# Kernel tuning notes

Hardware: AMD Instinct MI355X
Metric: run time of the kernel (lower is better)

The kernel has to match this reference:

```python
import jax, jax.numpy as jnp
import numpy as np

N_NODES = 50000
N_EDGES = 1048576
NODE_H = 128
EDGE_H = 64
GNN_H = 128


def setup_inputs() -> dict:
    key = jax.random.key(0)
    k = jax.random.split(key, 6)
    x = jax.random.normal(k[0], (N_NODES, NODE_H), dtype=jnp.float32)
    edge_index = jax.random.randint(k[1], (2, N_EDGES), 0, N_NODES, dtype=jnp.int64)
    edge_attr = jax.random.normal(k[2], (N_EDGES, EDGE_H), dtype=jnp.float32)
    # kaiming-ish init for the two Linear layers
    W1 = jax.random.normal(k[3], (2 * NODE_H + EDGE_H, GNN_H), dtype=jnp.float32) * (2.0 / (2 * NODE_H + EDGE_H)) ** 0.5
    b1 = jnp.zeros((GNN_H,), dtype=jnp.float32)
    W2 = jax.random.normal(k[4], (NODE_H + GNN_H, GNN_H), dtype=jnp.float32) * (2.0 / (NODE_H + GNN_H)) ** 0.5
    b2 = jnp.zeros((GNN_H,), dtype=jnp.float32)
    return {"x": x, "edge_index": edge_index, "edge_attr": edge_attr,
            "W1": W1, "b1": b1, "W2": W2, "b2": b2}


def reference(x, edge_index, edge_attr, W1, b1, W2, b2):
    # GroupGNN_Layer.forward
    row, col = edge_index[0], edge_index[1]
    n = x.shape[0]
    # gather + concat + edge MLP (Linear -> ReLU)
    msg = jnp.concatenate([x[row], x[col], edge_attr], axis=1)  # [E, 2*node_h+edge_h]
    msg = jax.nn.relu(msg @ W1 + b1)                            # [E, gnn_h]
    # scatter_mean over target nodes (col), dim_size = n
    s = jax.ops.segment_sum(msg, col, num_segments=n)           # [N, gnn_h]
    cnt = jax.ops.segment_sum(jnp.ones((msg.shape[0],), msg.dtype), col, num_segments=n)
    agg = s / jnp.maximum(cnt, 1.0)[:, None]                    # empty segments -> 0
    # node MLP (Linear -> ReLU)
    out = jax.nn.relu(jnp.concatenate([x, agg], axis=1) @ W2 + b2)  # [N, gnn_h]
    return out
```

## Files before the change

kernel.cpp:

```cpp
#include <hip/hip_runtime.h>
#include <hip/hip_bf16.h>
#include <stdint.h>

#define E_EDGES 1048576
#define NN 50000
#define NODE_H 128
#define EDGE_H 64
#define GNN_H 128
#define K1 320
#define K2 256
#define NB 16
#define NG (NN / NB)
#define CAPN 64

typedef __bf16 bf16_t;
typedef __bf16 bf16x8 __attribute__((ext_vector_type(8)));
typedef float floatx4 __attribute__((ext_vector_type(4)));

#define OFF_FLAG 0
#define OFF_CNT 256
#define OFF_W1T 213248
#define OFF_W2T 295168
#define OFF_W1ABT 360704
#define OFF_W1CT 426240
#define OFF_RC 442880
#define OFF_REC 26042880
#define WS_V13 ((size_t)OFF_REC + (size_t)NN * CAPN * 8)

__device__ __forceinline__ long load_idx(const void* ei, int is64, long off) {
    return is64 ? (long)((const long long*)ei)[off] : (long)((const int*)ei)[off];
}
__device__ __forceinline__ float bflo(unsigned u) {
    return __builtin_bit_cast(float, u << 16);
}
__device__ __forceinline__ float bfhi(unsigned u) {
    return __builtin_bit_cast(float, u & 0xffff0000u);
}

#define MFMA(a, b, c) __builtin_amdgcn_mfma_f32_16x16x32_bf16(a, b, c, 0, 0, 0)


__global__ __launch_bounds__(256) void prep_w(const float* __restrict__ W1,
                                              const float* __restrict__ W2,
                                              char* __restrict__ ws) {
    bf16_t* w2t = (bf16_t*)(ws + OFF_W2T);
    bf16_t* w1abt = (bf16_t*)(ws + OFF_W1ABT);
    bf16_t* w1ct = (bf16_t*)(ws + OFF_W1CT);
    int tid = blockIdx.x * 256 + threadIdx.x;
    int nt = 64 * 256;
    for (int i = tid; i < K2 * GNN_H; i += nt) {
        int n = i / K2, k = i - n * K2;
        w2t[i] = (bf16_t)W2[k * GNN_H + n];
    }
    for (int i = tid; i < 256 * 128; i += nt) {
        int n = i >> 7, k = i & 127;
        int kk = (n < 128) ? k : k + 128;
        w1abt[i] = (bf16_t)W1[kk * GNN_H + (n & 127)];
    }
    for (int i = tid; i < 128 * 64; i += nt) {
        int n = i >> 6, k = i & 63;
        w1ct[i] = (bf16_t)W1[(256 + k) * GNN_H + n];
    }
}

__global__ __launch_bounds__(256) void scatrc_kernel(const int* __restrict__ ei32,
                                                     const float* __restrict__ x,
                                                     char* __restrict__ ws,
                                                     int* __restrict__ cnt) {
    if (blockIdx.x < E_EDGES / 256) {
        __shared__ int nz;
        int tid = threadIdx.x;
        int e = blockIdx.x * 256 + tid;
        if (tid == 0) nz = 0;
        __syncthreads();
        if (ei32[2 * e + 1] != 0) atomicOr(&nz, 1);
        __syncthreads();
        int is64 = (nz == 0);
        const long long* e64 = (const long long*)ei32;
        int row = is64 ? (int)e64[e] : ei32[e];
        int col = is64 ? (int)e64[E_EDGES + e] : ei32[E_EDGES + e];
        int pos = atomicAdd(cnt + col, 1);
        if (pos < CAPN)
            ((unsigned long long*)(ws + OFF_REC))[((size_t)col << 6) + pos] =
                (unsigned long long)(unsigned)e |
                ((unsigned long long)(unsigned)row << 20);
    } else {
        const bf16_t* w1abt = (const bf16_t*)(ws + OFF_W1ABT);
        bf16_t* rc = (bf16_t*)(ws + OFF_RC);
        int lane = threadIdx.x & 63;
        int w = threadIdx.x >> 6;
        int li = lane & 15;
        int h = lane >> 4;
        int m0 = (blockIdx.x - E_EDGES / 256) * 16;

        bf16x8 bf[4][4];
#pragma unroll
        for (int t = 0; t < 4; ++t)
#pragma unroll
            for (int ks = 0; ks < 4; ++ks)
                bf[t][ks] = *(const bf16x8*)(w1abt + (w * 64 + t * 16 + li) * 128 + ks * 32 + h * 8);

        const float* px = x + (long)(m0 + li) * NODE_H + h * 8;
        floatx4 acc[4] = {{0.f, 0.f, 0.f, 0.f}, {0.f, 0.f, 0.f, 0.f},
                          {0.f, 0.f, 0.f, 0.f}, {0.f, 0.f, 0.f, 0.f}};
#pragma unroll
        for (int ks = 0; ks < 4; ++ks) {
            floatx4 f0 = *(const floatx4*)(px + ks * 32);
            floatx4 f1 = *(const floatx4*)(px + ks * 32 + 4);
            bf16x8 a;
#pragma unroll
            for (int j = 0; j < 4; ++j) {
                a[j] = (bf16_t)f0[j];
                a[j + 4] = (bf16_t)f1[j];
            }
#pragma unroll
            for (int t = 0; t < 4; ++t) acc[t] = MFMA(a, bf[t][ks], acc[t]);
        }
#pragma unroll
        for (int t = 0; t < 4; ++t) {
            int base = w * 64 + t * 16;
            int ppos;
            if (base < 128)
                ppos = (base >> 5) * 32 + li * 2 + ((base >> 4) & 1);
            else
                ppos = base + li;
#pragma unroll
            for (int r = 0; r < 4; ++r)
                rc[(long)(m0 + 4 * h + r) * 256 + ppos] = (bf16_t)acc[t][r];
        }
    }
}

__global__ __launch_bounds__(256) void fused_v14(
    const float* __restrict__ x, const float* __restrict__ ea,
    const float* __restrict__ b1, const float* __restrict__ b2,
    const char* __restrict__ ws, float* __restrict__ out) {
    const bf16_t* w1ct = (const bf16_t*)(ws + OFF_W1CT);
    const bf16_t* w2t = (const bf16_t*)(ws + OFF_W2T);
    const bf16_t* rc = (const bf16_t*)(ws + OFF_RC);
    const char* rcb = (const char*)rc;
    const int* cnt = (const int*)(ws + OFF_CNT);
    const unsigned long long* rec = (const unsigned long long*)(ws + OFF_REC);

    __shared__ float agg[NB][132];
    __shared__ float cl[NB][132];
    __shared__ int scnt[NB];
    __shared__ int offs[NB + 1];
    __shared__ unsigned lrec_e[NB * CAPN];
    __shared__ unsigned lrec_p[NB * CAPN];

    int tid = threadIdx.x;
    int lane = tid & 63;
    int w = tid >> 6;
    int li = lane & 15;
    int h = lane >> 4;
    int h4 = h * 4;
    int c0 = w * 32;
    int roff = w * 64 + li * 4;
    int v0 = blockIdx.x * NB;

    for (int i = tid; i < NB * 132; i += 256) ((float*)agg)[i] = 0.f;
    {
        int j = tid >> 4;
        int cc = (tid & 15) * 8;
        bf16x8 v = *(const bf16x8*)(rc + (long)(v0 + j) * 256 + 128 + cc);
#pragma unroll
        for (int q = 0; q < 8; ++q) cl[j][cc + q] = (float)v[q] + b1[cc + q];
    }
    if (tid < NB) {
        int c = cnt[v0 + tid];
        scnt[tid] = c > CAPN ? CAPN : c;
    }
    __syncthreads();
    if (tid == 0) {
        int run = 0;
#pragma unroll
        for (int j = 0; j < NB; ++j) {
            offs[j] = run;
            run += scnt[j];
        }
        offs[NB] = run;
    }
    __syncthreads();
    for (int flat = tid; flat < NB * CAPN; flat += 256) {
        int j = flat >> 6, i = flat & 63;
        if (i < scnt[j]) {
            unsigned long long r = rec[((size_t)(v0 + j) << 6) + i];
            int d = offs[j] + i;
            lrec_e[d] = (unsigned)r & 0xFFFFFu;
            lrec_p[d] = ((unsigned)(r >> 20) & 0x1FFFFu) | ((unsigned)j << 17);
        }
    }

    bf16x8 bc00 = *(const bf16x8*)(w1ct + (c0 + li) * 64 + h * 8);
    bf16x8 bc01 = *(const bf16x8*)(w1ct + (c0 + li) * 64 + 32 + h * 8);
    bf16x8 bc10 = *(const bf16x8*)(w1ct + (c0 + 16 + li) * 64 + h * 8);
    bf16x8 bc11 = *(const bf16x8*)(w1ct + (c0 + 16 + li) * 64 + 32 + h * 8);
    __syncthreads();

    int n_e = offs[NB];
    if (n_e > 0) {
        const int ntile = (n_e + 15) >> 4;
#define CP(p) ((p) < n_e ? (p) : n_e - 1)
#define DECL_SET(S)                                                     \
    unsigned pe##S, pk##S##0, pk##S##1, pk##S##2, pk##S##3, nlp##S;     \
    floatx4 ea##S##0, ea##S##1, ea##S##2, ea##S##3;                     \
    unsigned rp##S##0, rp##S##1, rp##S##2, rp##S##3;
#define IDX(S, T)                                                       \
    do {                                                                \
        int bb_ = (T) << 4;                                             \
        pe##S = lrec_e[CP(bb_ + li)];                                   \
        pk##S##0 = lrec_p[CP(bb_ + h4)];                                \
        pk##S##1 = lrec_p[CP(bb_ + h4 + 1)];                            \
        pk##S##2 = lrec_p[CP(bb_ + h4 + 2)];                            \
        pk##S##3 = lrec_p[CP(bb_ + h4 + 3)];                            \
    } while (0)
#define DATA(S)                                                         \
    do {                                                                \
        const float* pe_ = ea + (size_t)pe##S * EDGE_H + h * 8;         \
        ea##S##0 = *(const floatx4*)(pe_);                              \
        ea##S##1 = *(const floatx4*)(pe_ + 4);                          \
        ea##S##2 = *(const floatx4*)(pe_ + 32);                         \
        ea##S##3 = *(const floatx4*)(pe_ + 36);                         \
        rp##S##0 = *(const unsigned*)(rcb + (((size_t)(pk##S##0 & 0x1FFFFu)) << 9) + roff); \
        rp##S##1 = *(const unsigned*)(rcb + (((size_t)(pk##S##1 & 0x1FFFFu)) << 9) + roff); \
        rp##S##2 = *(const unsigned*)(rcb + (((size_t)(pk##S##2 & 0x1FFFFu)) << 9) + roff); \
        rp##S##3 = *(const unsigned*)(rcb + (((size_t)(pk##S##3 & 0x1FFFFu)) << 9) + roff); \
        nlp##S = ((pk##S##0 >> 17) & 15u) | (((pk##S##1 >> 17) & 15u) << 4) | \
                 (((pk##S##2 >> 17) & 15u) << 8) |                      \
                 (((pk##S##3 >> 17) & 15u) << 12);                      \
    } while (0)
#define COMPUTE(S, T)                                                   \
    do {                                                                \
        bf16x8 a0_, a1_;                                                \
        _Pragma("unroll") for (int j_ = 0; j_ < 4; ++j_) {              \
            a0_[j_] = (bf16_t)ea##S##0[j_];                             \
            a0_[j_ + 4] = (bf16_t)ea##S##1[j_];                         \
            a1_[j_] = (bf16_t)ea##S##2[j_];                             \
            a1_[j_ + 4] = (bf16_t)ea##S##3[j_];                         \
        }                                                               \
        floatx4 ac0_ = {0.f, 0.f, 0.f, 0.f};                            \
        floatx4 ac1_ = {0.f, 0.f, 0.f, 0.f};                            \
        ac0_ = MFMA(a0_, bc00, ac0_);                                   \
        ac0_ = MFMA(a1_, bc01, ac0_);                                   \
        ac1_ = MFMA(a0_, bc10, ac1_);                                   \
        ac1_ = MFMA(a1_, bc11, ac1_);                                   \
        int base_ = (T) << 4;                                           \
        int nl0_ = (int)(nlp##S & 15u);                                 \
        int nl1_ = (int)((nlp##S >> 4) & 15u);                          \
        int nl2_ = (int)((nlp##S >> 8) & 15u);                          \
        int nl3_ = (int)((nlp##S >> 12) & 15u);                         \
        float m00_ = fmaxf(ac0_[0] + bflo(rp##S##0) + cl[nl0_][c0 + li], 0.f); \
        float m01_ = fmaxf(ac0_[1] + bflo(rp##S##1) + cl[nl1_][c0 + li], 0.f); \
        float m02_ = fmaxf(ac0_[2] + bflo(rp##S##2) + cl[nl2_][c0 + li], 0.f); \
        float m03_ = fmaxf(ac0_[3] + bflo(rp##S##3) + cl[nl3_][c0 + li], 0.f); \
        float m10_ = fmaxf(ac1_[0] + bfhi(rp##S##0) + cl[nl0_][c0 + 16 + li], 0.f); \
        float m11_ = fmaxf(ac1_[1] + bfhi(rp##S##1) + cl[nl1_][c0 + 16 + li], 0.f); \
        float m12_ = fmaxf(ac1_[2] + bfhi(rp##S##2) + cl[nl2_][c0 + 16 + li], 0.f); \
        float m13_ = fmaxf(ac1_[3] + bfhi(rp##S##3) + cl[nl3_][c0 + 16 + li], 0.f); \
        if ((base_ + h4 + 3) < n_e && nl0_ == nl3_) {                   \
            atomicAdd(&agg[nl0_][c0 + li], m00_ + m01_ + m02_ + m03_);  \
            atomicAdd(&agg[nl0_][c0 + 16 + li], m10_ + m11_ + m12_ + m13_); \
        } else {                                                        \
            if (base_ + h4 < n_e) {                                     \
                atomicAdd(&agg[nl0_][c0 + li], m00_);                   \
                atomicAdd(&agg[nl0_][c0 + 16 + li], m10_);              \
            }                                                           \
            if (base_ + h4 + 1 < n_e) {                                 \
                atomicAdd(&agg[nl1_][c0 + li], m01_);                   \
                atomicAdd(&agg[nl1_][c0 + 16 + li], m11_);              \
            }                                                           \
            if (base_ + h4 + 2 < n_e) {                                 \
                atomicAdd(&agg[nl2_][c0 + li], m02_);                   \
                atomicAdd(&agg[nl2_][c0 + 16 + li], m12_);              \
            }                                                           \
            if (base_ + h4 + 3 < n_e) {                                 \
                atomicAdd(&agg[nl3_][c0 + li], m03_);                   \
                atomicAdd(&agg[nl3_][c0 + 16 + li], m13_);              \
            }                                                           \
        }                                                               \
    } while (0)

        DECL_SET(A)
        DECL_SET(B)
        IDX(A, 0);
        IDX(B, 1);
        DATA(A);
        DATA(B);
        IDX(A, 2);
        IDX(B, 3);
        for (int t = 0; t < ntile; t += 2) {
            COMPUTE(A, t);
            DATA(A);
            IDX(A, t + 4);
            COMPUTE(B, t + 1);
            DATA(B);
            IDX(B, t + 5);
        }
#undef CP
    }
    __syncthreads();

    bf16x8 bfr2[2][8];
#pragma unroll
    for (int t = 0; t < 2; ++t)
#pragma unroll
        for (int ks = 0; ks < 8; ++ks)
            bfr2[t][ks] = *(const bf16x8*)(w2t + (long)(c0 + t * 16 + li) * K2 + ks * 32 + h * 8);
    float nb0 = b2[c0 + li];
    float nb1 = b2[c0 + 16 + li];

    int node = v0 + li;
    float rcn = 1.0f / fmaxf((float)cnt[node], 1.0f);
    const float* px = x + (long)node * NODE_H + h * 8;
    floatx4 acc0 = {0.f, 0.f, 0.f, 0.f};
    floatx4 acc1 = {0.f, 0.f, 0.f, 0.f};
#pragma unroll
    for (int ks = 0; ks < 8; ++ks) {
        floatx4 f0, f1;
        if (ks < 4) {
            f0 = *(const floatx4*)(px + ks * 32);
            f1 = *(const floatx4*)(px + ks * 32 + 4);
        } else {
            const float* sa = &agg[li][(ks - 4) * 32 + h * 8];
            f0 = *(const floatx4*)(sa);
            f1 = *(const floatx4*)(sa + 4);
            f0 *= rcn;
            f1 *= rcn;
        }
        bf16x8 a;
#pragma unroll
        for (int j = 0; j < 4; ++j) {
            a[j] = (bf16_t)f0[j];
            a[j + 4] = (bf16_t)f1[j];
        }
        acc0 = MFMA(a, bfr2[0][ks], acc0);
        acc1 = MFMA(a, bfr2[1][ks], acc1);
    }
#pragma unroll
    for (int r = 0; r < 4; ++r) {
        long ir = v0 + h4 + r;
        out[ir * GNN_H + c0 + li] = fmaxf(acc0[r] + nb0, 0.f);
        out[ir * GNN_H + c0 + 16 + li] = fmaxf(acc1[r] + nb1, 0.f);
    }
}


__global__ void prep_kernel(const float* __restrict__ W1, const float* __restrict__ W2,
                            const int* __restrict__ ei32, char* __restrict__ ws) {
    bf16_t* w1t = (bf16_t*)(ws + OFF_W1T);
    bf16_t* w2t = (bf16_t*)(ws + OFF_W2T);
    int tid = blockIdx.x * blockDim.x + threadIdx.x;
    int nt = gridDim.x * blockDim.x;
    for (int i = tid; i < K1 * GNN_H; i += nt) {
        int n = i / K1, k = i - n * K1;
        w1t[i] = (bf16_t)W1[k * GNN_H + n];
    }
    for (int i = tid; i < K2 * GNN_H; i += nt) {
        int n = i / K2, k = i - n * K2;
        w2t[i] = (bf16_t)W2[k * GNN_H + n];
    }
    if (blockIdx.x == 0) {
        __shared__ int any_nonzero;
        if (threadIdx.x == 0) any_nonzero = 0;
        __syncthreads();
        if (ei32[2 * threadIdx.x + 1] != 0) atomicOr(&any_nonzero, 1);
        __syncthreads();
        if (threadIdx.x == 0) *(int*)(ws + OFF_FLAG) = (any_nonzero == 0) ? 1 : 0;
    }
}

__global__ void count_kernel(const void* __restrict__ ei, const char* __restrict__ ws,
                             float* __restrict__ cnt) {
    int is64 = *(const int*)(ws + OFF_FLAG);
    int e = blockIdx.x * blockDim.x + threadIdx.x;
    if (e < E_EDGES) {
        long c = load_idx(ei, is64, (long)E_EDGES + e);
        atomicAdd(cnt + c, 1.0f);
    }
}

__global__ __launch_bounds__(256) void edge_kernel(
    const float* __restrict__ x, const void* __restrict__ ei,
    const float* __restrict__ ea, const float* __restrict__ b1,
    const char* __restrict__ ws, float* __restrict__ s) {
    const bf16_t* w1t = (const bf16_t*)(ws + OFF_W1T);
    int is64 = *(const int*)(ws + OFF_FLAG);
    int lane = threadIdx.x & 63;
    int w = threadIdx.x >> 6;
    int li = lane & 15;
    int h = lane >> 4;
    int n0 = w * 32;

    bf16x8 bf[2][10];
#pragma unroll
    for (int t = 0; t < 2; ++t)
#pragma unroll
        for (int ks = 0; ks < 10; ++ks)
            bf[t][ks] = *(const bf16x8*)(w1t + (long)(n0 + t * 16 + li) * K1 + ks * 32 + h * 8);
    float bias0 = b1[n0 + li];
    float bias1 = b1[n0 + 16 + li];

    const int ntiles = E_EDGES / 16;
    for (int tile = blockIdx.x; tile < ntiles; tile += gridDim.x) {
        int m0 = tile * 16;
        int e = m0 + li;
        long rowi = load_idx(ei, is64, e);
        long coli = load_idx(ei, is64, (long)E_EDGES + e);
        const float* pr = x + rowi * NODE_H + h * 8;
        const float* pc = x + coli * NODE_H + h * 8;
        const float* pe = ea + (long)e * EDGE_H + h * 8;
        floatx4 acc0 = {0.f, 0.f, 0.f, 0.f};
        floatx4 acc1 = {0.f, 0.f, 0.f, 0.f};
#pragma unroll
        for (int ks = 0; ks < 10; ++ks) {
            const float* src = (ks < 4) ? (pr + ks * 32) : (ks < 8) ? (pc + (ks - 4) * 32)
                                                                    : (pe + (ks - 8) * 32);
            floatx4 f0 = *(const floatx4*)(src);
            floatx4 f1 = *(const floatx4*)(src + 4);
            bf16x8 a;
#pragma unroll
            for (int j = 0; j < 4; ++j) {
                a[j] = (bf16_t)f0[j];
                a[j + 4] = (bf16_t)f1[j];
            }
            acc0 = MFMA(a, bf[0][ks], acc0);
            acc1 = MFMA(a, bf[1][ks], acc1);
        }
        long cols[4];
#pragma unroll
        for (int r = 0; r < 4; ++r)
            cols[r] = load_idx(ei, is64, (long)E_EDGES + m0 + h * 4 + r);
#pragma unroll
        for (int r = 0; r < 4; ++r) {
            float v0 = fmaxf(acc0[r] + bias0, 0.f);
            float v1 = fmaxf(acc1[r] + bias1, 0.f);
            atomicAdd(s + cols[r] * GNN_H + n0 + li, v0);
            atomicAdd(s + cols[r] * GNN_H + n0 + 16 + li, v1);
        }
    }
}

__global__ __launch_bounds__(256) void node_kernel(
    const float* __restrict__ x, const float* __restrict__ b2,
    const char* __restrict__ ws, const float* __restrict__ cnt,
    const float* __restrict__ s, float* __restrict__ out) {
    const bf16_t* w2t = (const bf16_t*)(ws + OFF_W2T);
    int lane = threadIdx.x & 63;
    int w = threadIdx.x >> 6;
    int li = lane & 15;
    int h = lane >> 4;
    int n0 = w * 32;

    bf16x8 bf[2][8];
#pragma unroll
    for (int t = 0; t < 2; ++t)
#pragma unroll
        for (int ks = 0; ks < 8; ++ks)
            bf[t][ks] = *(const bf16x8*)(w2t + (long)(n0 + t * 16 + li) * K2 + ks * 32 + h * 8);
    float bias0 = b2[n0 + li];
    float bias1 = b2[n0 + 16 + li];

    int m0 = blockIdx.x * 16;
    int i = m0 + li;
    float rcn = 1.0f / fmaxf(cnt[i], 1.0f);
    const float* px = x + (long)i * NODE_H + h * 8;
    const float* ps = s + (long)i * GNN_H + h * 8;
    floatx4 acc0 = {0.f, 0.f, 0.f, 0.f};
    floatx4 acc1 = {0.f, 0.f, 0.f, 0.f};
#pragma unroll
    for (int ks = 0; ks < 8; ++ks) {
        const float* src = (ks < 4) ? (px + ks * 32) : (ps + (ks - 4) * 32);
        floatx4 f0 = *(const floatx4*)(src);
        floatx4 f1 = *(const floatx4*)(src + 4);
        if (ks >= 4) {
            f0 *= rcn;
            f1 *= rcn;
        }
        bf16x8 a;
#pragma unroll
        for (int j = 0; j < 4; ++j) {
            a[j] = (bf16_t)f0[j];
            a[j + 4] = (bf16_t)f1[j];
        }
        acc0 = MFMA(a, bf[0][ks], acc0);
        acc1 = MFMA(a, bf[1][ks], acc1);
    }
    __syncthreads();
#pragma unroll
    for (int r = 0; r < 4; ++r) {
        long ir = m0 + h * 4 + r;
        out[ir * GNN_H + n0 + li] = fmaxf(acc0[r] + bias0, 0.f);
        out[ir * GNN_H + n0 + 16 + li] = fmaxf(acc1[r] + bias1, 0.f);
    }
}

extern "C" void kernel_launch(void* const* d_in, const int* in_sizes, int n_in,
                              void* d_out, int out_size, void* d_ws, size_t ws_size,
                              hipStream_t stream) {
    const float* x = (const float*)d_in[0];
    const void* ei = d_in[1];
    const float* ea = (const float*)d_in[2];
    const float* W1 = (const float*)d_in[3];
    const float* b1 = (const float*)d_in[4];
    const float* W2 = (const float*)d_in[5];
    const float* b2 = (const float*)d_in[6];
    float* out = (float*)d_out;
    char* ws = (char*)d_ws;

    if (ws_size >= WS_V13) {
        int* cnt = (int*)(ws + OFF_CNT);
        hipMemsetAsync(cnt, 0, NN * 4, stream);
        prep_w<<<64, 256, 0, stream>>>(W1, W2, ws);
        scatrc_kernel<<<E_EDGES / 256 + NG, 256, 0, stream>>>((const int*)ei, x, ws, cnt);
        fused_v14<<<NG, 256, 0, stream>>>(x, ea, b1, b2, ws, out);
    } else {
        prep_kernel<<<32, 256, 0, stream>>>(W1, W2, (const int*)ei, ws);
        float* cntf = (float*)(ws + OFF_CNT);
        hipMemsetAsync(cntf, 0, NN * 4, stream);
        hipMemsetAsync(out, 0, (size_t)NN * GNN_H * 4, stream);
        count_kernel<<<E_EDGES / 256, 256, 0, stream>>>(ei, ws, cntf);
        edge_kernel<<<4096, 256, 0, stream>>>(x, ei, ea, b1, ws, out);
        node_kernel<<<NN / 16, 256, 0, stream>>>(x, b2, ws, cntf, out, out);
    }
}
```

Baseline: 408.6 us.

## Stream edge attributes into LDS via direct global-to-LDS loads with ring buffer

Replaces per-lane register loads of edge_attr rows with __builtin_amdgcn_global_load_lds into a four-slot shared-memory ring, staged four tiles ahead. Reads go back out of LDS with a rotated column layout to avoid bank conflicts. This is meant to cut vector register pressure and issue more loads in flight for the random-gather edge stream. In exchange it adds two workgroup barriers per tile and hand-set vmcnt waits, which depend on the exact count of outstanding loads and are fragile.

```diff
diff --git a/kernel.cpp b/kernel.cpp
--- a/kernel.cpp
+++ b/kernel.cpp
@@ -131,7 +131,7 @@
     }
 }
 
-__global__ __launch_bounds__(256) void fused_v14(
+__global__ __launch_bounds__(256) void fused_v15(
     const float* __restrict__ x, const float* __restrict__ ea,
     const float* __restrict__ b1, const float* __restrict__ b2,
     const char* __restrict__ ws, float* __restrict__ out) {
@@ -148,6 +148,7 @@
     __shared__ int offs[NB + 1];
     __shared__ unsigned lrec_e[NB * CAPN];
     __shared__ unsigned lrec_p[NB * CAPN];
+    __shared__ float eabuf[4][16][64];
 
     int tid = threadIdx.x;
     int lane = tid & 63;
@@ -201,55 +202,56 @@
     int n_e = offs[NB];
     if (n_e > 0) {
         const int ntile = (n_e + 15) >> 4;
-#define CP(p) ((p) < n_e ? (p) : n_e - 1)
-#define DECL_SET(S)                                                     \
-    unsigned pe##S, pk##S##0, pk##S##1, pk##S##2, pk##S##3, nlp##S;     \
-    floatx4 ea##S##0, ea##S##1, ea##S##2, ea##S##3;                     \
-    unsigned rp##S##0, rp##S##1, rp##S##2, rp##S##3;
-#define IDX(S, T)                                                       \
-    do {                                                                \
-        int bb_ = (T) << 4;                                             \
-        pe##S = lrec_e[CP(bb_ + li)];                                   \
-        pk##S##0 = lrec_p[CP(bb_ + h4)];                                \
-        pk##S##1 = lrec_p[CP(bb_ + h4 + 1)];                            \
-        pk##S##2 = lrec_p[CP(bb_ + h4 + 2)];                            \
-        pk##S##3 = lrec_p[CP(bb_ + h4 + 3)];                            \
+        int jj = (w << 2) + (lane >> 4);
+        unsigned ebrot = (unsigned)(((lane & 15) * 16 + ((jj & 7) << 5)) & 255);
+        int c0r = ((h << 3) - ((li & 7) << 3)) & 63;
+        int c1r = (c0r + 32) & 63;
+
+#define CPm(p) ((p) < 0 ? 0 : ((p) < n_e ? (p) : n_e - 1))
+#define DECL_SET(S) unsigned rp##S##0, rp##S##1, rp##S##2, rp##S##3, nlp##S;
+#define STAGE(T)                                                            \
+    do {                                                                    \
+        unsigned e_ = lrec_e[CPm(((T) << 4) + jj)];                         \
+        const char* g_ = (const char*)ea + ((size_t)e_ << 8) + ebrot;       \
+        __builtin_amdgcn_global_load_lds(                                   \
+            (const __attribute__((address_space(1))) void*)g_,              \
+            (__attribute__((address_space(3))) void*)&eabuf[(T) & 3][w << 2][0], \
+            16, 0, 0);                                                      \
     } while (0)
-#define DATA(S)                                                         \
-    do {                                                                \
-        const float* pe_ = ea + (size_t)pe##S * EDGE_H + h * 8;         \
-        ea##S##0 = *(const floatx4*)(pe_);                              \
-        ea##S##1 = *(const floatx4*)(pe_ + 4);                          \
-        ea##S##2 = *(const floatx4*)(pe_ + 32);                         \
-        ea##S##3 = *(const floatx4*)(pe_ + 36);                         \
-        rp##S##0 = *(const unsigned*)(rcb + (((size_t)(pk##S##0 & 0x1FFFFu)) << 9) + roff); \
-        rp##S##1 = *(const unsigned*)(rcb + (((size_t)(pk##S##1 & 0x1FFFFu)) << 9) + roff); \
-        rp##S##2 = *(const unsigned*)(rcb + (((size_t)(pk##S##2 & 0x1FFFFu)) << 9) + roff); \
-        rp##S##3 = *(const unsigned*)(rcb + (((size_t)(pk##S##3 & 0x1FFFFu)) << 9) + roff); \
-        nlp##S = ((pk##S##0 >> 17) & 15u) | (((pk##S##1 >> 17) & 15u) << 4) | \
-                 (((pk##S##2 >> 17) & 15u) << 8) |                      \
-                 (((pk##S##3 >> 17) & 15u) << 12);                      \
+#define DATA_R(S, T)                                                        \
+    do {                                                                    \
+        int bb_ = (T) << 4;                                                 \
+        unsigned k0_ = lrec_p[CPm(bb_ + h4)];                               \
+        unsigned k1_ = lrec_p[CPm(bb_ + h4 + 1)];                           \
+        unsigned k2_ = lrec_p[CPm(bb_ + h4 + 2)];                           \
+        unsigned k3_ = lrec_p[CPm(bb_ + h4 + 3)];                           \
+        rp##S##0 = *(const unsigned*)(rcb + (((size_t)(k0_ & 0x1FFFFu)) << 9) + roff); \
+        rp##S##1 = *(const unsigned*)(rcb + (((size_t)(k1_ & 0x1FFFFu)) << 9) + roff); \
+        rp##S##2 = *(const unsigned*)(rcb + (((size_t)(k2_ & 0x1FFFFu)) << 9) + roff); \
+        rp##S##3 = *(const unsigned*)(rcb + (((size_t)(k3_ & 0x1FFFFu)) << 9) + roff); \
+        nlp##S = ((k0_ >> 17) & 15u) | (((k1_ >> 17) & 15u) << 4) |         \
+                 (((k2_ >> 17) & 15u) << 8) | (((k3_ >> 17) & 15u) << 12);  \
     } while (0)
-#define COMPUTE(S, T)                                                   \
-    do {                                                                \
-        bf16x8 a0_, a1_;                                                \
-        _Pragma("unroll") for (int j_ = 0; j_ < 4; ++j_) {              \
-            a0_[j_] = (bf16_t)ea##S##0[j_];                             \
-            a0_[j_ + 4] = (bf16_t)ea##S##1[j_];                         \
-            a1_[j_] = (bf16_t)ea##S##2[j_];                             \
-            a1_[j_ + 4] = (bf16_t)ea##S##3[j_];                         \
-        }                                                               \
-        floatx4 ac0_ = {0.f, 0.f, 0.f, 0.f};                            \
-        floatx4 ac1_ = {0.f, 0.f, 0.f, 0.f};                            \
-        ac0_ = MFMA(a0_, bc00, ac0_);                                   \
-        ac0_ = MFMA(a1_, bc01, ac0_);                                   \
-        ac1_ = MFMA(a0_, bc10, ac1_);                                   \
-        ac1_ = MFMA(a1_, bc11, ac1_);                                   \
-        int base_ = (T) << 4;                                           \
-        int nl0_ = (int)(nlp##S & 15u);                                 \
-        int nl1_ = (int)((nlp##S >> 4) & 15u);                          \
-        int nl2_ = (int)((nlp##S >> 8) & 15u);                          \
-        int nl3_ = (int)((nlp##S >> 12) & 15u);                         \
+#define COMPUTE(S, T, F0, F1, F2, F3)                                       \
+    do {                                                                    \
+        bf16x8 a0_, a1_;                                                    \
+        _Pragma("unroll") for (int j_ = 0; j_ < 4; ++j_) {                  \
+            a0_[j_] = (bf16_t)F0[j_];                                       \
+            a0_[j_ + 4] = (bf16_t)F1[j_];                                   \
+            a1_[j_] = (bf16_t)F2[j_];                                       \
+            a1_[j_ + 4] = (bf16_t)F3[j_];                                   \
+        }                                                                   \
+        floatx4 ac0_ = {0.f, 0.f, 0.f, 0.f};                                \
+        floatx4 ac1_ = {0.f, 0.f, 0.f, 0.f};                                \
+        ac0_ = MFMA(a0_, bc00, ac0_);                                       \
+        ac0_ = MFMA(a1_, bc01, ac0_);                                       \
+        ac1_ = MFMA(a0_, bc10, ac1_);                                       \
+        ac1_ = MFMA(a1_, bc11, ac1_);                                       \
+        int base_ = (T) << 4;                                               \
+        int nl0_ = (int)(nlp##S & 15u);                                     \
+        int nl1_ = (int)((nlp##S >> 4) & 15u);                              \
+        int nl2_ = (int)((nlp##S >> 8) & 15u);                              \
+        int nl3_ = (int)((nlp##S >> 12) & 15u);                             \
         float m00_ = fmaxf(ac0_[0] + bflo(rp##S##0) + cl[nl0_][c0 + li], 0.f); \
         float m01_ = fmaxf(ac0_[1] + bflo(rp##S##1) + cl[nl1_][c0 + li], 0.f); \
         float m02_ = fmaxf(ac0_[2] + bflo(rp##S##2) + cl[nl2_][c0 + li], 0.f); \
@@ -258,46 +260,53 @@
         float m11_ = fmaxf(ac1_[1] + bfhi(rp##S##1) + cl[nl1_][c0 + 16 + li], 0.f); \
         float m12_ = fmaxf(ac1_[2] + bfhi(rp##S##2) + cl[nl2_][c0 + 16 + li], 0.f); \
         float m13_ = fmaxf(ac1_[3] + bfhi(rp##S##3) + cl[nl3_][c0 + 16 + li], 0.f); \
-        if ((base_ + h4 + 3) < n_e && nl0_ == nl3_) {                   \
-            atomicAdd(&agg[nl0_][c0 + li], m00_ + m01_ + m02_ + m03_);  \
+        if ((base_ + h4 + 3) < n_e && nl0_ == nl3_) {                       \
+            atomicAdd(&agg[nl0_][c0 + li], m00_ + m01_ + m02_ + m03_);      \
             atomicAdd(&agg[nl0_][c0 + 16 + li], m10_ + m11_ + m12_ + m13_); \
-        } else {                                                        \
-            if (base_ + h4 < n_e) {                                     \
-                atomicAdd(&agg[nl0_][c0 + li], m00_);                   \
-                atomicAdd(&agg[nl0_][c0 + 16 + li], m10_);              \
-            }                                                           \
-            if (base_ + h4 + 1 < n_e) {                                 \
-                atomicAdd(&agg[nl1_][c0 + li], m01_);                   \
-                atomicAdd(&agg[nl1_][c0 + 16 + li], m11_);              \
-            }                                                           \
-            if (base_ + h4 + 2 < n_e) {                                 \
-                atomicAdd(&agg[nl2_][c0 + li], m02_);                   \
-                atomicAdd(&agg[nl2_][c0 + 16 + li], m12_);              \
-            }                                                           \
-            if (base_ + h4 + 3 < n_e) {                                 \
-                atomicAdd(&agg[nl3_][c0 + li], m03_);                   \
-                atomicAdd(&agg[nl3_][c0 + 16 + li], m13_);              \
-            }                                                           \
-        }                                                               \
+        } else {                                                            \
+            if (base_ + h4 < n_e) {                                         \
+                atomicAdd(&agg[nl0_][c0 + li], m00_);                       \
+                atomicAdd(&agg[nl0_][c0 + 16 + li], m10_);                  \
+            }                                                               \
+            if (base_ + h4 + 1 < n_e) {                                     \
+                atomicAdd(&agg[nl1_][c0 + li], m01_);                       \
+                atomicAdd(&agg[nl1_][c0 + 16 + li], m11_);                  \
+            }                                                               \
+            if (base_ + h4 + 2 < n_e) {                                     \
+                atomicAdd(&agg[nl2_][c0 + li], m02_);                       \
+                atomicAdd(&agg[nl2_][c0 + 16 + li], m12_);                  \
+            }                                                               \
+            if (base_ + h4 + 3 < n_e) {                                     \
+                atomicAdd(&agg[nl3_][c0 + li], m03_);                       \
+                atomicAdd(&agg[nl3_][c0 + 16 + li], m13_);                  \
+            }                                                               \
+        }                                                                   \
+    } while (0)
+#define HALF(S, TT)                                                         \
+    do {                                                                    \
+        asm volatile("s_waitcnt vmcnt(19)" ::: "memory");                   \
+        __builtin_amdgcn_s_barrier();                                       \
+        __builtin_amdgcn_sched_barrier(0);                                  \
+        const float* rp_ = &eabuf[(TT) & 3][li][0];                         \
+        floatx4 f0_ = *(const floatx4*)(rp_ + c0r);                         \
+        floatx4 f1_ = *(const floatx4*)(rp_ + c0r + 4);                     \
+        floatx4 f2_ = *(const floatx4*)(rp_ + c1r);                         \
+        floatx4 f3_ = *(const floatx4*)(rp_ + c1r + 4);                     \
+        asm volatile("s_waitcnt lgkmcnt(0)" ::: "memory");                  \
+        __builtin_amdgcn_sched_barrier(0);                                  \
+        __builtin_amdgcn_s_barrier();                                       \
+        STAGE((TT) + 4);                                                    \
+        if ((TT) >= 0) COMPUTE(S, TT, f0_, f1_, f2_, f3_);                  \
+        DATA_R(S, (TT) + 2);                                                \
     } while (0)
 
         DECL_SET(A)
         DECL_SET(B)
-        IDX(A, 0);
-        IDX(B, 1);
-        DATA(A);
-        DATA(B);
-        IDX(A, 2);
-        IDX(B, 3);
-        for (int t = 0; t < ntile; t += 2) {
-            COMPUTE(A, t);
-            DATA(A);
-            IDX(A, t + 4);
-            COMPUTE(B, t + 1);
-            DATA(B);
-            IDX(B, t + 5);
-        }
-#undef CP
+        for (int t = -4; t < ntile; t += 2) {
+            HALF(A, t);
+            HALF(B, t + 1);
+        }
+#undef CPm
     }
     __syncthreads();
 
@@ -513,7 +522,7 @@
         hipMemsetAsync(cnt, 0, NN * 4, stream);
         prep_w<<<64, 256, 0, stream>>>(W1, W2, ws);
         scatrc_kernel<<<E_EDGES / 256 + NG, 256, 0, stream>>>((const int*)ei, x, ws, cnt);
-        fused_v14<<<NG, 256, 0, stream>>>(x, ea, b1, b2, ws, out);
+        fused_v15<<<NG, 256, 0, stream>>>(x, ea, b1, b2, ws, out);
     } else {
         prep_kernel<<<32, 256, 0, stream>>>(W1, W2, (const int*)ei, ws);
         float* cntf = (float*)(ws + OFF_CNT);
```

Result: slower. 497.1 us (+21.6%).

## Build CSR via histogram+scan and pre-sort edge_attr as bf16 by target

Applied to the files above, without the earlier changes.

Replaces the fixed-capacity per-node bucket (64 slots) with a proper CSR: a histogram pass, a single-block prefix scan, then a scatter that writes row indices and a bf16 copy of edge_attr in target-sorted order. The fused kernel then reads edge attributes contiguously as bf16 instead of gathering fp32 rows by edge id, and finds each edge's local node by binary search over offsets. This adds an extra histogram pass over the edge list, a serial single-block scan, and a full extra write and read of the bf16 edge attributes.

```diff
diff --git a/kernel.cpp b/kernel.cpp
--- a/kernel.cpp
+++ b/kernel.cpp
@@ -11,7 +11,7 @@
 #define K2 256
 #define NB 16
 #define NG (NN / NB)
-#define CAPN 64
+#define LCAP 1024
 
 typedef __bf16 bf16_t;
 typedef __bf16 bf16x8 __attribute__((ext_vector_type(8)));
@@ -19,13 +19,16 @@
 
 #define OFF_FLAG 0
 #define OFF_CNT 256
-#define OFF_W1T 213248
-#define OFF_W2T 295168
-#define OFF_W1ABT 360704
-#define OFF_W1CT 426240
-#define OFF_RC 442880
-#define OFF_REC 26042880
-#define WS_V13 ((size_t)OFF_REC + (size_t)NN * CAPN * 8)
+#define OFF_RP 200448
+#define OFF_WOFF 400640
+#define OFF_W2T 600832
+#define OFF_W1ABT 666368
+#define OFF_W1CT 731904
+#define OFF_W1T 748288
+#define OFF_RC 830464
+#define OFF_ROW 26430464
+#define OFF_EAB 30624768
+#define WS_V16 ((size_t)OFF_EAB + (size_t)E_EDGES * 128)
 
 __device__ __forceinline__ long load_idx(const void* ei, int is64, long off) {
     return is64 ? (long)((const long long*)ei)[off] : (long)((const int*)ei)[off];
@@ -40,33 +43,79 @@
 #define MFMA(a, b, c) __builtin_amdgcn_mfma_f32_16x16x32_bf16(a, b, c, 0, 0, 0)
 
 
-__global__ __launch_bounds__(256) void prep_w(const float* __restrict__ W1,
-                                              const float* __restrict__ W2,
-                                              char* __restrict__ ws) {
+__global__ __launch_bounds__(256) void prep_hist(const float* __restrict__ W1,
+                                                 const float* __restrict__ W2,
+                                                 const int* __restrict__ ei32,
+                                                 char* __restrict__ ws,
+                                                 int* __restrict__ cnt) {
+    __shared__ int nz;
+    int tid = threadIdx.x;
+    int gid = blockIdx.x * 256 + tid;
+    if (tid == 0) nz = 0;
+    __syncthreads();
+    if (ei32[2 * gid + 1] != 0) atomicOr(&nz, 1);
+    __syncthreads();
+    int is64 = (nz == 0);
+
     bf16_t* w2t = (bf16_t*)(ws + OFF_W2T);
     bf16_t* w1abt = (bf16_t*)(ws + OFF_W1ABT);
     bf16_t* w1ct = (bf16_t*)(ws + OFF_W1CT);
-    int tid = blockIdx.x * 256 + threadIdx.x;
-    int nt = 64 * 256;
-    for (int i = tid; i < K2 * GNN_H; i += nt) {
-        int n = i / K2, k = i - n * K2;
-        w2t[i] = (bf16_t)W2[k * GNN_H + n];
-    }
-    for (int i = tid; i < 256 * 128; i += nt) {
-        int n = i >> 7, k = i & 127;
+    if (gid < K2 * GNN_H) {
+        int n = gid / K2, k = gid - n * K2;
+        w2t[gid] = (bf16_t)W2[k * GNN_H + n];
+    }
+    if (gid < 256 * 128) {
+        int n = gid >> 7, k = gid & 127;
         int kk = (n < 128) ? k : k + 128;
-        w1abt[i] = (bf16_t)W1[kk * GNN_H + (n & 127)];
-    }
-    for (int i = tid; i < 128 * 64; i += nt) {
-        int n = i >> 6, k = i & 63;
-        w1ct[i] = (bf16_t)W1[(256 + k) * GNN_H + n];
-    }
+        w1abt[gid] = (bf16_t)W1[kk * GNN_H + (n & 127)];
+    }
+    if (gid < 128 * 64) {
+        int n = gid >> 6, k = gid & 63;
+        w1ct[gid] = (bf16_t)W1[(256 + k) * GNN_H + n];
+    }
+    if (gid == 0) *(int*)(ws + OFF_FLAG) = is64;
+
+    const long long* e64 = (const long long*)ei32;
+    for (int e = gid; e < E_EDGES; e += 2048 * 256) {
+        int col = is64 ? (int)e64[E_EDGES + e] : ei32[E_EDGES + e];
+        atomicAdd(cnt + col, 1);
+    }
+}
+
+__global__ __launch_bounds__(1024) void scan_kernel(const int* __restrict__ cnt,
+                                                    int* __restrict__ rowptr,
+                                                    int* __restrict__ woff) {
+    __shared__ int part[1024];
+    int t = threadIdx.x;
+    const int CH = (NN + 1023) / 1024;
+    int base = t * CH;
+    int n = NN - base;
+    if (n < 0) n = 0;
+    if (n > CH) n = CH;
+    int s = 0;
+    for (int i = 0; i < n; ++i) s += cnt[base + i];
+    part[t] = s;
+    __syncthreads();
+    for (int off = 1; off < 1024; off <<= 1) {
+        int v = (t >= off) ? part[t - off] : 0;
+        __syncthreads();
+        part[t] += v;
+        __syncthreads();
+    }
+    int run = part[t] - s;
+    for (int i = 0; i < n; ++i) {
+        rowptr[base + i] = run;
+        woff[base + i] = run;
+        run += cnt[base + i];
+    }
+    if (t == 1023) rowptr[NN] = part[1023];
 }
 
 __global__ __launch_bounds__(256) void scatrc_kernel(const int* __restrict__ ei32,
+                                                     const float* __restrict__ ea,
                                                      const float* __restrict__ x,
                                                      char* __restrict__ ws,
-                                                     int* __restrict__ cnt) {
+                                                     int* __restrict__ woff) {
     if (blockIdx.x < E_EDGES / 256) {
         __shared__ int nz;
         int tid = threadIdx.x;
@@ -79,11 +128,22 @@
         const long long* e64 = (const long long*)ei32;
         int row = is64 ? (int)e64[e] : ei32[e];
         int col = is64 ? (int)e64[E_EDGES + e] : ei32[E_EDGES + e];
-        int pos = atomicAdd(cnt + col, 1);
-        if (pos < CAPN)
-            ((unsigned long long*)(ws + OFF_REC))[((size_t)col << 6) + pos] =
-                (unsigned long long)(unsigned)e |
-                ((unsigned long long)(unsigned)row << 20);
+        int pos = atomicAdd(woff + col, 1);
+        ((unsigned*)(ws + OFF_ROW))[pos] = (unsigned)row;
+        const floatx4* src = (const floatx4*)(ea + (size_t)e * EDGE_H);
+        bf16_t* dst = (bf16_t*)(ws + OFF_EAB) + ((size_t)pos << 6);
+#pragma unroll
+        for (int c = 0; c < 8; ++c) {
+            floatx4 f0 = src[2 * c];
+            floatx4 f1 = src[2 * c + 1];
+            bf16x8 v;
+#pragma unroll
+            for (int j = 0; j < 4; ++j) {
+                v[j] = (bf16_t)f0[j];
+                v[j + 4] = (bf16_t)f1[j];
+            }
+            *(bf16x8*)(dst + c * 8) = v;
+        }
     } else {
         const bf16_t* w1abt = (const bf16_t*)(ws + OFF_W1ABT);
         bf16_t* rc = (bf16_t*)(ws + OFF_RC);
@@ -131,23 +191,22 @@
     }
 }
 
-__global__ __launch_bounds__(256) void fused_v14(
-    const float* __restrict__ x, const float* __restrict__ ea,
-    const float* __restrict__ b1, const float* __restrict__ b2,
-    const char* __restrict__ ws, float* __restrict__ out) {
+__global__ __launch_bounds__(256) void fused_v16(
+    const float* __restrict__ x, const float* __restrict__ b1,
+    const float* __restrict__ b2, const char* __restrict__ ws,
+    float* __restrict__ out) {
     const bf16_t* w1ct = (const bf16_t*)(ws + OFF_W1CT);
     const bf16_t* w2t = (const bf16_t*)(ws + OFF_W2T);
     const bf16_t* rc = (const bf16_t*)(ws + OFF_RC);
     const char* rcb = (const char*)rc;
-    const int* cnt = (const int*)(ws + OFF_CNT);
-    const unsigned long long* rec = (const unsigned long long*)(ws + OFF_REC);
+    const int* rowptr = (const int*)(ws + OFF_RP);
+    const unsigned* row32 = (const unsigned*)(ws + OFF_ROW);
+    const bf16_t* eab = (const bf16_t*)(ws + OFF_EAB);
 
     __shared__ float agg[NB][132];
     __shared__ float cl[NB][132];
-    __shared__ int scnt[NB];
     __shared__ int offs[NB + 1];
-    __shared__ unsigned lrec_e[NB * CAPN];
-    __shared__ unsigned lrec_p[NB * CAPN];
+    __shared__ unsigned lrec_p[LCAP];
 
     int tid = threadIdx.x;
     int lane = tid & 63;
@@ -167,29 +226,20 @@
 #pragma unroll
         for (int q = 0; q < 8; ++q) cl[j][cc + q] = (float)v[q] + b1[cc + q];
     }
-    if (tid < NB) {
-        int c = cnt[v0 + tid];
-        scnt[tid] = c > CAPN ? CAPN : c;
-    }
-    __syncthreads();
-    if (tid == 0) {
-        int run = 0;
-#pragma unroll
-        for (int j = 0; j < NB; ++j) {
-            offs[j] = run;
-            run += scnt[j];
-        }
-        offs[NB] = run;
-    }
-    __syncthreads();
-    for (int flat = tid; flat < NB * CAPN; flat += 256) {
-        int j = flat >> 6, i = flat & 63;
-        if (i < scnt[j]) {
-            unsigned long long r = rec[((size_t)(v0 + j) << 6) + i];
-            int d = offs[j] + i;
-            lrec_e[d] = (unsigned)r & 0xFFFFFu;
-            lrec_p[d] = ((unsigned)(r >> 20) & 0x1FFFFu) | ((unsigned)j << 17);
-        }
+    if (tid <= NB) offs[tid] = rowptr[v0 + tid];
+    __syncthreads();
+    int e_beg = offs[0];
+    int n_e = offs[NB] - e_beg;
+    if (n_e > LCAP) n_e = LCAP;
+    for (int d = tid; d < n_e; d += 256) {
+        unsigned r = row32[e_beg + d];
+        int dd = e_beg + d;
+        int j = 0;
+        if (dd >= offs[j + 8]) j += 8;
+        if (dd >= offs[j + 4]) j += 4;
+        if (dd >= offs[j + 2]) j += 2;
+        if (dd >= offs[j + 1]) j += 1;
+        lrec_p[d] = (r & 0x1FFFFu) | ((unsigned)j << 17);
     }
 
     bf16x8 bc00 = *(const bf16x8*)(w1ct + (c0 + li) * 64 + h * 8);
@@ -198,30 +248,27 @@
     bf16x8 bc11 = *(const bf16x8*)(w1ct + (c0 + 16 + li) * 64 + 32 + h * 8);
     __syncthreads();
 
-    int n_e = offs[NB];
     if (n_e > 0) {
         const int ntile = (n_e + 15) >> 4;
 #define CP(p) ((p) < n_e ? (p) : n_e - 1)
 #define DECL_SET(S)                                                     \
-    unsigned pe##S, pk##S##0, pk##S##1, pk##S##2, pk##S##3, nlp##S;     \
-    floatx4 ea##S##0, ea##S##1, ea##S##2, ea##S##3;                     \
+    unsigned pk##S##0, pk##S##1, pk##S##2, pk##S##3, nlp##S;            \
+    bf16x8 ealo##S, eahi##S;                                            \
     unsigned rp##S##0, rp##S##1, rp##S##2, rp##S##3;
 #define IDX(S, T)                                                       \
     do {                                                                \
         int bb_ = (T) << 4;                                             \
-        pe##S = lrec_e[CP(bb_ + li)];                                   \
         pk##S##0 = lrec_p[CP(bb_ + h4)];                                \
         pk##S##1 = lrec_p[CP(bb_ + h4 + 1)];                            \
         pk##S##2 = lrec_p[CP(bb_ + h4 + 2)];                            \
         pk##S##3 = lrec_p[CP(bb_ + h4 + 3)];                            \
     } while (0)
-#define DATA(S)                                                         \
+#define DATA(S, T)                                                      \
     do {                                                                \
-        const float* pe_ = ea + (size_t)pe##S * EDGE_H + h * 8;         \
-        ea##S##0 = *(const floatx4*)(pe_);                              \
-        ea##S##1 = *(const floatx4*)(pe_ + 4);                          \
-        ea##S##2 = *(const floatx4*)(pe_ + 32);                         \
-        ea##S##3 = *(const floatx4*)(pe_ + 36);                         \
+        int bb_ = (T) << 4;                                             \
+        const bf16_t* pe_ = eab + ((size_t)(e_beg + CP(bb_ + li)) << 6); \
+        ealo##S = *(const bf16x8*)(pe_ + h * 8);                        \
+        eahi##S = *(const bf16x8*)(pe_ + 32 + h * 8);                   \
         rp##S##0 = *(const unsigned*)(rcb + (((size_t)(pk##S##0 & 0x1FFFFu)) << 9) + roff); \
         rp##S##1 = *(const unsigned*)(rcb + (((size_t)(pk##S##1 & 0x1FFFFu)) << 9) + roff); \
         rp##S##2 = *(const unsigned*)(rcb + (((size_t)(pk##S##2 & 0x1FFFFu)) << 9) + roff); \
@@ -232,19 +279,12 @@
     } while (0)
 #define COMPUTE(S, T)                                                   \
     do {                                                                \
-        bf16x8 a0_, a1_;                                                \
-        _Pragma("unroll") for (int j_ = 0; j_ < 4; ++j_) {              \
-            a0_[j_] = (bf16_t)ea##S##0[j_];                             \
-            a0_[j_ + 4] = (bf16_t)ea##S##1[j_];                         \
-            a1_[j_] = (bf16_t)ea##S##2[j_];                             \
-            a1_[j_ + 4] = (bf16_t)ea##S##3[j_];                         \
-        }                                                               \
         floatx4 ac0_ = {0.f, 0.f, 0.f, 0.f};                            \
         floatx4 ac1_ = {0.f, 0.f, 0.f, 0.f};                            \
-        ac0_ = MFMA(a0_, bc00, ac0_);                                   \
-        ac0_ = MFMA(a1_, bc01, ac0_);                                   \
-        ac1_ = MFMA(a0_, bc10, ac1_);                                   \
-        ac1_ = MFMA(a1_, bc11, ac1_);                                   \
+        ac0_ = MFMA(ealo##S, bc00, ac0_);                               \
+        ac0_ = MFMA(eahi##S, bc01, ac0_);                               \
+        ac1_ = MFMA(ealo##S, bc10, ac1_);                               \
+        ac1_ = MFMA(eahi##S, bc11, ac1_);                               \
         int base_ = (T) << 4;                                           \
         int nl0_ = (int)(nlp##S & 15u);                                 \
         int nl1_ = (int)((nlp##S >> 4) & 15u);                          \
@@ -285,16 +325,16 @@
         DECL_SET(B)
         IDX(A, 0);
         IDX(B, 1);
-        DATA(A);
-        DATA(B);
+        DATA(A, 0);
+        DATA(B, 1);
         IDX(A, 2);
         IDX(B, 3);
         for (int t = 0; t < ntile; t += 2) {
             COMPUTE(A, t);
-            DATA(A);
+            DATA(A, t + 2);
             IDX(A, t + 4);
             COMPUTE(B, t + 1);
-            DATA(B);
+            DATA(B, t + 3);
             IDX(B, t + 5);
         }
 #undef CP
@@ -311,7 +351,7 @@
     float nb1 = b2[c0 + 16 + li];
 
     int node = v0 + li;
-    float rcn = 1.0f / fmaxf((float)cnt[node], 1.0f);
+    float rcn = 1.0f / fmaxf((float)(rowptr[node + 1] - rowptr[node]), 1.0f);
     const float* px = x + (long)node * NODE_H + h * 8;
     floatx4 acc0 = {0.f, 0.f, 0.f, 0.f};
     floatx4 acc1 = {0.f, 0.f, 0.f, 0.f};
@@ -508,12 +548,14 @@
     float* out = (float*)d_out;
     char* ws = (char*)d_ws;
 
-    if (ws_size >= WS_V13) {
+    if (ws_size >= WS_V16) {
         int* cnt = (int*)(ws + OFF_CNT);
         hipMemsetAsync(cnt, 0, NN * 4, stream);
-        prep_w<<<64, 256, 0, stream>>>(W1, W2, ws);
-        scatrc_kernel<<<E_EDGES / 256 + NG, 256, 0, stream>>>((const int*)ei, x, ws, cnt);
-        fused_v14<<<NG, 256, 0, stream>>>(x, ea, b1, b2, ws, out);
+        prep_hist<<<2048, 256, 0, stream>>>(W1, W2, (const int*)ei, ws, cnt);
+        scan_kernel<<<1, 1024, 0, stream>>>(cnt, (int*)(ws + OFF_RP), (int*)(ws + OFF_WOFF));
+        scatrc_kernel<<<E_EDGES / 256 + NG, 256, 0, stream>>>(
+            (const int*)ei, ea, x, ws, (int*)(ws + OFF_WOFF));
+        fused_v16<<<NG, 256, 0, stream>>>(x, b1, b2, ws, out);
     } else {
         prep_kernel<<<32, 256, 0, stream>>>(W1, W2, (const int*)ei, ws);
         float* cntf = (float*)(ws + OFF_CNT);
```

Result: slower. 590.5 us (+44.5%).
